# Performance work log

Measured on AMD Instinct MI355X. Metric: run time of the kernel, lower is better.

Reference implementation:

```python
import jax, jax.numpy as jnp
import numpy as np

LN_EPS = 1e-12


def setup_inputs() -> dict:
    key = jax.random.key(0)
    ks = jax.random.split(key, 10)
    B, S, W, D, H = 16, 512, 5, 200, 768
    std = 0.02
    return {
        "layer_output": jax.random.normal(ks[0], (B, S, H), dtype=jnp.float32),
        "word_embeddings": jax.random.normal(ks[1], (B, S, W, D), dtype=jnp.float32),
        "word_mask": jax.random.randint(ks[2], (B, S, W), 0, 2, dtype=jnp.int64),
        "W1": jax.random.normal(ks[3], (D, H), dtype=jnp.float32) * std,
        "b1": jnp.zeros((H,), dtype=jnp.float32),
        "W2": jax.random.normal(ks[4], (H, H), dtype=jnp.float32) * std,
        "b2": jnp.zeros((H,), dtype=jnp.float32),
        "attn_W": jax.random.normal(ks[5], (H, H), dtype=jnp.float32) * std,
        "ln_gamma": jnp.ones((H,), dtype=jnp.float32),
        "ln_beta": jnp.zeros((H,), dtype=jnp.float32),
    }


def reference(layer_output, word_embeddings, word_mask, W1, b1, W2, b2, attn_W, ln_gamma, ln_beta):
    # word_transform: Linear -> Tanh -> Linear (dropout = identity in eval)
    we = jnp.tanh(jnp.einsum("bswd,dh->bswh", word_embeddings, W1) + b1)
    we = jnp.einsum("bswh,hk->bswk", we, W2) + b2  # [B,S,W,H]

    # bilinear word attention: (x @ attn_W) . word_outputs -> score over W
    q = jnp.einsum("bsh,hk->bsk", layer_output, attn_W)  # [B,S,H]
    alpha = jnp.einsum("bsk,bswk->bsw", q, we)            # [B,S,W]
    alpha = alpha + (1.0 - word_mask.astype(alpha.dtype)) * -10000.0
    alpha = jax.nn.softmax(alpha, axis=-1)

    # weighted sum over words + residual
    agg = jnp.einsum("bsw,bswh->bsh", alpha, we)
    h = layer_output + agg

    # LayerNorm (fuse_layer; dropout = identity in eval)
    mu = jnp.mean(h, axis=-1, keepdims=True)
    var = jnp.mean(jnp.square(h - mu), axis=-1, keepdims=True)
    return (h - mu) * jax.lax.rsqrt(var + LN_EPS) * ln_gamma + ln_beta
```

## Files before the change

### kernel.cpp

```cpp
#include <hip/hip_runtime.h>
#include <hip/hip_bf16.h>
#include <math.h>


typedef __attribute__((ext_vector_type(8))) short bf16x8;
typedef __attribute__((ext_vector_type(4))) float f32x4;

__device__ __forceinline__ unsigned short f2bf_bits(float f) {
    __hip_bfloat16 h = __float2bfloat16(f);
    return *reinterpret_cast<unsigned short*>(&h);
}
__device__ __forceinline__ float bf_bits2f(unsigned short u) {
    union { unsigned int i; float f; } v; v.i = ((unsigned int)u) << 16; return v.f;
}
__device__ __forceinline__ float tanh_fast(float x) {
    float xc = fminf(fmaxf(x, -9.f), 9.f);
    float t  = __expf(2.f * xc);
    return (t - 1.f) * __builtin_amdgcn_rcpf(t + 1.f);
}
__device__ __forceinline__ bf16x8 pack8(float4 a, float4 b) {
    union { bf16x8 v; unsigned short s[8]; } u;
    u.s[0]=f2bf_bits(a.x); u.s[1]=f2bf_bits(a.y); u.s[2]=f2bf_bits(a.z); u.s[3]=f2bf_bits(a.w);
    u.s[4]=f2bf_bits(b.x); u.s[5]=f2bf_bits(b.y); u.s[6]=f2bf_bits(b.z); u.s[7]=f2bf_bits(b.w);
    return u.v;
}

__device__ __forceinline__ void async_cp16(const void* g, void* lds) {
#if __has_builtin(__builtin_amdgcn_global_load_lds)
    auto gp = (const __attribute__((address_space(1))) unsigned int*)g;
    auto lp = (__attribute__((address_space(3))) unsigned int*)lds;
    __builtin_amdgcn_global_load_lds(gp, lp, 16, 0, 0);
#else
    *(uint4*)lds = *(const uint4*)g;
#endif
}

__device__ __forceinline__ void sched_fence()  { asm volatile("" ::: "memory"); }
__device__ __forceinline__ void wait8_barrier(){ asm volatile("s_waitcnt vmcnt(8)\ns_barrier" ::: "memory"); }
__device__ __forceinline__ void wait0_barrier(){ asm volatile("s_waitcnt vmcnt(0)\ns_barrier" ::: "memory"); }
__device__ __forceinline__ void barrier_only() { asm volatile("s_barrier" ::: "memory"); }

template<bool F32SRC, bool HAS_BIAS, bool TANH_ACT, bool RESID, bool OUT_BF16,
         int N, int K, int KREAL>
__device__ __forceinline__ void gemm_body(
    const void* __restrict__ Ap, const void* __restrict__ Btp,
    const float* __restrict__ bias, const float* __restrict__ resid,
    void* __restrict__ outp, int m0, int n0, unsigned char* smem)
{
    constexpr int NIT = K / 64;
    const int tid  = threadIdx.x;
    const int lane = tid & 63;
    const int wave = tid >> 6;
    const int wm   = wave & 1;
    const int wn   = wave >> 1;
    const int row16 = lane & 15;
    const int kq    = lane >> 4;

    f32x4 acc[4][4];
#pragma unroll
    for (int i = 0; i < 4; i++)
#pragma unroll
        for (int j = 0; j < 4; j++) acc[i][j] = (f32x4){0.f, 0.f, 0.f, 0.f};

    auto compute_tile = [&](const unsigned short* As, const unsigned short* Bs, bool full) {
        bf16x8 af[2][4], bg[2][4];
#pragma unroll
        for (int mi = 0; mi < 4; mi++) {
            const int r = wm * 64 + mi * 16 + row16;
            af[0][mi] = *(const bf16x8*)&As[r * 64 + (kq ^ (r & 7)) * 8];
            if (full) af[1][mi] = *(const bf16x8*)&As[r * 64 + ((4 + kq) ^ (r & 7)) * 8];
        }
#pragma unroll
        for (int ni = 0; ni < 4; ni++) {
            const int r = wn * 64 + ni * 16 + row16;
            bg[0][ni] = *(const bf16x8*)&Bs[r * 64 + (kq ^ (r & 7)) * 8];
            if (full) bg[1][ni] = *(const bf16x8*)&Bs[r * 64 + ((4 + kq) ^ (r & 7)) * 8];
        }
        __builtin_amdgcn_s_setprio(1);
#pragma unroll
        for (int mi = 0; mi < 4; mi++)
#pragma unroll
            for (int ni = 0; ni < 4; ni++)
                acc[mi][ni] = __builtin_amdgcn_mfma_f32_16x16x32_bf16(
                    af[0][mi], bg[0][ni], acc[mi][ni], 0, 0, 0);
        if (full) {
#pragma unroll
            for (int mi = 0; mi < 4; mi++)
#pragma unroll
                for (int ni = 0; ni < 4; ni++)
                    acc[mi][ni] = __builtin_amdgcn_mfma_f32_16x16x32_bf16(
                        af[1][mi], bg[1][ni], acc[mi][ni], 0, 0, 0);
        }
        __builtin_amdgcn_s_setprio(0);
    };

    if constexpr (F32SRC) {
        const float* A32 = (const float*)Ap;
        const float* B32 = (const float*)Btp;
        unsigned short* As = (unsigned short*)smem;
        unsigned short* Bs = As + 8192;
        for (int t = 0; t < NIT; ++t) {
#pragma unroll
            for (int i = 0; i < 4; ++i) {
                const int c = i * 256 + tid;
                const int row = c >> 3, sl = c & 7;
                const int kcc = sl ^ (row & 7);
                const float* sa = A32 + (size_t)(m0 + row) * K + t * 64 + kcc * 8;
                *(bf16x8*)&As[row * 64 + sl * 8] = pack8(*(const float4*)sa, *(const float4*)(sa + 4));
                const float* sb = B32 + (size_t)(n0 + row) * K + t * 64 + kcc * 8;
                *(bf16x8*)&Bs[row * 64 + sl * 8] = pack8(*(const float4*)sb, *(const float4*)(sb + 4));
            }
            __syncthreads();
            compute_tile(As, Bs, true);
            __syncthreads();
        }
    } else {
        const __hip_bfloat16* A  = (const __hip_bfloat16*)Ap;
        const __hip_bfloat16* Bt = (const __hip_bfloat16*)Btp;
        const int rsub = lane >> 3;
        const int slot = lane & 7;
        const int kc   = slot ^ rsub;
        const __hip_bfloat16* gA = A  + (size_t)(m0 + wave * 32 + rsub) * K + kc * 8;
        const __hip_bfloat16* gB = Bt + (size_t)(n0 + wave * 32 + rsub) * K + kc * 8;
        unsigned short* lA0 = (unsigned short*)smem + wave * 2048 + lane * 8;
        unsigned short* lB0 = lA0 + 8192;

        auto stage = [&](int t, int buf) {
            unsigned short* lA = lA0 + buf * 16384;
            unsigned short* lB = lB0 + buf * 16384;
            const __hip_bfloat16* a = gA + t * 64;
            const __hip_bfloat16* b = gB + t * 64;
#pragma unroll
            for (int i = 0; i < 4; i++) {
                async_cp16(a + (size_t)(8 * i) * K, lA + i * 512);
                async_cp16(b + (size_t)(8 * i) * K, lB + i * 512);
            }
            sched_fence();
        };

        stage(0, 0);
        if (NIT > 1) stage(1, 1);
#pragma unroll
        for (int t = 0; t < NIT; ++t) {
            if (t == NIT - 1) wait0_barrier(); else wait8_barrier();
            const unsigned short* As = (const unsigned short*)(smem + (t & 1) * 32768);
            const unsigned short* Bs = As + 8192;
            compute_tile(As, Bs, (t * 64 + 32 < KREAL));
            barrier_only();
            if (t + 2 < NIT) stage(t + 2, t & 1);
        }
    }

    if (OUT_BF16) {
        unsigned short* rep = (unsigned short*)smem;
#pragma unroll
        for (int ni = 0; ni < 4; ni++) {
            const int c = wn * 64 + ni * 16 + row16;
            float bcol = HAS_BIAS ? bias[n0 + c] : 0.f;
#pragma unroll
            for (int mi = 0; mi < 4; mi++)
#pragma unroll
                for (int r = 0; r < 4; r++) {
                    const int rr = wm * 64 + mi * 16 + kq * 4 + r;
                    float v = acc[mi][ni][r];
                    if (HAS_BIAS) v += bcol;
                    if (TANH_ACT) v = tanh_fast(v);
                    rep[rr * 132 + c] = f2bf_bits(v);
                }
        }
        __syncthreads();
#pragma unroll
        for (int p = 0; p < 8; p++) {
            const int lin = p * 256 + tid;
            const int row = lin >> 4;
            const int c8  = lin & 15;
            const unsigned short* s = &rep[row * 132 + c8 * 8];
            union { uint4 u; unsigned long long q[2]; } d;
            d.q[0] = *(const unsigned long long*)(s);
            d.q[1] = *(const unsigned long long*)(s + 4);
            *(uint4*)((__hip_bfloat16*)outp + (size_t)(m0 + row) * N + n0 + c8 * 8) = d.u;
        }
    } else {
        float* rep = (float*)smem;
#pragma unroll
        for (int h = 0; h < 2; h++) {
            if (wm == h) {
#pragma unroll
                for (int ni = 0; ni < 4; ni++) {
                    const int c = wn * 64 + ni * 16 + row16;
                    float bcol = HAS_BIAS ? bias[n0 + c] : 0.f;
#pragma unroll
                    for (int mi = 0; mi < 4; mi++)
#pragma unroll
                        for (int r = 0; r < 4; r++) {
                            const int rr = mi * 16 + kq * 4 + r;
                            float v = acc[mi][ni][r];
                            if (HAS_BIAS) v += bcol;
                            if (TANH_ACT) v = tanh_fast(v);
                            rep[rr * 132 + c] = v;
                        }
                }
            }
            __syncthreads();
#pragma unroll
            for (int p = 0; p < 8; p++) {
                const int lin = p * 256 + tid;
                const int row = lin >> 5;
                const int c4  = lin & 31;
                float4 v = *(const float4*)&rep[row * 132 + c4 * 4];
                const int grow = m0 + h * 64 + row;
                if (RESID) {
                    float4 rv = *(const float4*)&resid[(size_t)grow * N + n0 + c4 * 4];
                    v.x += rv.x; v.y += rv.y; v.z += rv.z; v.w += rv.w;
                }
                *(float4*)((float*)outp + (size_t)grow * N + n0 + c4 * 4) = v;
            }
            __syncthreads();
        }
    }
}

template<bool HAS_BIAS, bool TANH_ACT, bool RESID, bool OUT_BF16, int N, int K, int GX>
__global__ __launch_bounds__(256) void mfma_gemm(
    const __hip_bfloat16* __restrict__ A,
    const __hip_bfloat16* __restrict__ Bt,
    const float* __restrict__ bias,
    const float* __restrict__ resid,
    void* __restrict__ outp)
{
    __shared__ __align__(16) unsigned char smem[65536];
    int bx, by;
    {
        const int total = gridDim.x;
        const int per_xcd = total >> 3;
        if ((total & 7) == 0 && (per_xcd % GX) == 0) {
            int xcd = blockIdx.x & 7, idx = blockIdx.x >> 3;
            int lin = xcd * per_xcd + idx;
            by = lin / GX; bx = lin % GX;
        } else { by = blockIdx.x / GX; bx = blockIdx.x % GX; }
    }
    gemm_body<false, HAS_BIAS, TANH_ACT, RESID, OUT_BF16, N, K, K>(
        A, Bt, bias, resid, outp, by * 128, bx * 128, smem);
}

__global__ __launch_bounds__(256) void tp_kernel(
    const __hip_bfloat16* __restrict__ Eb,  const __hip_bfloat16* __restrict__ W1Tb,
    const float* __restrict__ b1,           __hip_bfloat16* __restrict__ Tb,
    const __hip_bfloat16* __restrict__ xb,  const __hip_bfloat16* __restrict__ Ctb,
    __hip_bfloat16* __restrict__ Pb)
{
    __shared__ __align__(16) unsigned char smem[65536];
    if (blockIdx.x < 1920) {
        const int xcd = blockIdx.x & 7, idx = blockIdx.x >> 3;
        const int lin = xcd * 240 + idx;
        gemm_body<false, true, true, false, true, 768, 256, 224>(
            Eb, W1Tb, b1, nullptr, Tb, (lin / 6) * 128, (lin % 6) * 128, smem);
    } else {
        const int idq = blockIdx.x - 1920;
        const int xcd = idq & 7, idx = idq >> 3;
        const int lin = xcd * 48 + idx;
        gemm_body<false, false, false, false, true, 768, 768, 768>(
            xb, Ctb, nullptr, nullptr, Pb, (lin / 6) * 128, (lin % 6) * 128, smem);
    }
}

__global__ __launch_bounds__(256) void prep_kernel(
    const float* __restrict__ x,  __hip_bfloat16* __restrict__ xb,
    const float* __restrict__ w2,
    const float* __restrict__ aw,
    const float* __restrict__ E,  __hip_bfloat16* __restrict__ Eb,
    const float* __restrict__ W1, __hip_bfloat16* __restrict__ W1Tb,
    __hip_bfloat16* __restrict__ W2Tb,
    __hip_bfloat16* __restrict__ Ctb)
{
    __shared__ __align__(16) unsigned char smem[33792];
    float (*tile)[33] = (float(*)[33])smem;
    const int b = blockIdx.x, tid = threadIdx.x;
    if (b < 36) {
        gemm_body<true, false, false, false, true, 768, 768, 768>(
            w2, aw, nullptr, nullptr, Ctb, (b / 6) * 128, (b % 6) * 128, smem);
    } else if (b < 804) {
        const float* in; __hip_bfloat16* outb; int R, C, Rpad, t;
        if (b < 228) { t = b - 36;  in = W1; outb = W1Tb; R = 200; C = 768; Rpad = 256; }
        else         { t = b - 228; in = w2; outb = W2Tb; R = 768; C = 768; Rpad = 768; }
        const int c0 = (t % 24) * 32, r0 = (t / 24) * 32;
        const int xx = tid & 31, yy = tid >> 5;
#pragma unroll
        for (int i = 0; i < 32; i += 8) {
            int r = r0 + yy + i;
            tile[yy + i][xx] = (r < R) ? in[(size_t)r * C + c0 + xx] : 0.f;
        }
        __syncthreads();
#pragma unroll
        for (int i = 0; i < 32; i += 8)
            outb[(size_t)(c0 + yy + i) * Rpad + r0 + xx] = __float2bfloat16(tile[xx][yy + i]);
    } else if (b < 1572) {
        const long long base = (long long)(b - 804) * 2048 + tid;
        float4 v[8];
#pragma unroll
        for (int j = 0; j < 8; j++) v[j] = ((const float4*)x)[base + j * 256];
#pragma unroll
        for (int j = 0; j < 8; j++)
            ((ushort4*)xb)[base + j * 256] =
                make_ushort4(f2bf_bits(v[j].x), f2bf_bits(v[j].y), f2bf_bits(v[j].z), f2bf_bits(v[j].w));
    } else {
        const int lane = tid & 63, wave = tid >> 6;
        const long long r0 = (long long)(b - 1572) * 32 + wave * 8;
        const int k = lane * 4;
        float4 v[8];
#pragma unroll
        for (int j = 0; j < 8; j++) {
            v[j] = make_float4(0.f, 0.f, 0.f, 0.f);
            if (k < 200) v[j] = *(const float4*)&E[(r0 + j) * 200 + k];
        }
#pragma unroll
        for (int j = 0; j < 8; j++)
            *(ushort4*)&Eb[(r0 + j) * 256 + k] =
                make_ushort4(f2bf_bits(v[j].x), f2bf_bits(v[j].y), f2bf_bits(v[j].z), f2bf_bits(v[j].w));
    }
}

__global__ __launch_bounds__(256) void attn_kernel(
    const __hip_bfloat16* __restrict__ T,
    const __hip_bfloat16* P,
    const int* __restrict__ mask,
    __hip_bfloat16* S)
{
    const int lane = threadIdx.x & 63;
    const int wave = threadIdx.x >> 6;
    const int r    = blockIdx.x * 4 + wave;
    const int base = lane * 12;

    float pv[12];
    {
        const ushort4* pp = (const ushort4*)((const unsigned short*)P + (size_t)r * 768 + base);
        ushort4 u0 = pp[0], u1 = pp[1], u2 = pp[2];
        unsigned short us[12] = {u0.x,u0.y,u0.z,u0.w, u1.x,u1.y,u1.z,u1.w, u2.x,u2.y,u2.z,u2.w};
#pragma unroll
        for (int j = 0; j < 12; j++) pv[j] = bf_bits2f(us[j]);
    }
    float tv[5][12], part[5];
#pragma unroll
    for (int w = 0; w < 5; w++) {
        const ushort4* tp = (const ushort4*)((const unsigned short*)T + ((size_t)r * 5 + w) * 768 + base);
        ushort4 u0 = tp[0], u1 = tp[1], u2 = tp[2];
        unsigned short us[12] = {u0.x,u0.y,u0.z,u0.w, u1.x,u1.y,u1.z,u1.w, u2.x,u2.y,u2.z,u2.w};
        float s = 0.f;
#pragma unroll
        for (int j = 0; j < 12; j++) { tv[w][j] = bf_bits2f(us[j]); s += tv[w][j] * pv[j]; }
        part[w] = s;
    }
#pragma unroll
    for (int off = 32; off > 0; off >>= 1)
#pragma unroll
        for (int w = 0; w < 5; w++)
            part[w] += __shfl_xor(part[w], off, 64);

    float logit[5], mx = -1e30f;
#pragma unroll
    for (int w = 0; w < 5; w++) {
        float m = (float)mask[(size_t)r * 5 + w];
        logit[w] = part[w] - 10000.0f * (1.0f - m);
        mx = fmaxf(mx, logit[w]);
    }
    float se = 0.f;
#pragma unroll
    for (int w = 0; w < 5; w++) { logit[w] = expf(logit[w] - mx); se += logit[w]; }
    const float inv = 1.0f / se;

    unsigned short os[12];
#pragma unroll
    for (int j = 0; j < 12; j++) {
        float s = 0.f;
#pragma unroll
        for (int w = 0; w < 5; w++) s += logit[w] * tv[w][j];
        os[j] = f2bf_bits(s * inv);
    }
    ushort4* sp = (ushort4*)((unsigned short*)S + (size_t)r * 768 + base);
    sp[0] = make_ushort4(os[0], os[1], os[2],  os[3]);
    sp[1] = make_ushort4(os[4], os[5], os[6],  os[7]);
    sp[2] = make_ushort4(os[8], os[9], os[10], os[11]);
}

__global__ __launch_bounds__(256) void ln_kernel(
    const float* __restrict__ Hbuf, const float* __restrict__ gamma,
    const float* __restrict__ beta, float* __restrict__ out)
{
    const int lane = threadIdx.x & 63;
    const int wave = threadIdx.x >> 6;
    const int r    = blockIdx.x * 4 + wave;
    const float* hr = Hbuf + (size_t)r * 768 + lane * 12;

    float v[12];
    {
        float4 a = *(const float4*)(hr);
        float4 b = *(const float4*)(hr + 4);
        float4 c = *(const float4*)(hr + 8);
        v[0]=a.x; v[1]=a.y; v[2]=a.z; v[3]=a.w;
        v[4]=b.x; v[5]=b.y; v[6]=b.z; v[7]=b.w;
        v[8]=c.x; v[9]=c.y; v[10]=c.z; v[11]=c.w;
    }
    float s = 0.f;
#pragma unroll
    for (int j = 0; j < 12; j++) s += v[j];
#pragma unroll
    for (int off = 32; off > 0; off >>= 1) s += __shfl_xor(s, off, 64);
    const float mu = s * (1.f / 768.f);
    float vs = 0.f;
#pragma unroll
    for (int j = 0; j < 12; j++) { float d = v[j] - mu; vs += d * d; }
#pragma unroll
    for (int off = 32; off > 0; off >>= 1) vs += __shfl_xor(vs, off, 64);
    const float rs = rsqrtf(vs * (1.f / 768.f) + 1e-12f);

    float o[12];
#pragma unroll
    for (int j = 0; j < 12; j++) {
        int h = lane * 12 + j;
        o[j] = (v[j] - mu) * rs * gamma[h] + beta[h];
    }
    float* orow = out + (size_t)r * 768 + lane * 12;
    *(float4*)(orow)     = make_float4(o[0], o[1], o[2],  o[3]);
    *(float4*)(orow + 4) = make_float4(o[4], o[5], o[6],  o[7]);
    *(float4*)(orow + 8) = make_float4(o[8], o[9], o[10], o[11]);
}

extern "C" void kernel_launch(void* const* d_in, const int* in_sizes, int n_in,
                              void* d_out, int out_size, void* d_ws, size_t ws_size,
                              hipStream_t stream)
{
    const float* x      = (const float*)d_in[0];
    const float* E      = (const float*)d_in[1];
    const int*   mask   = (const int*)d_in[2];
    const float* W1     = (const float*)d_in[3];
    const float* b1     = (const float*)d_in[4];
    const float* W2     = (const float*)d_in[5];
    const float* b2     = (const float*)d_in[6];
    const float* attn_W = (const float*)d_in[7];
    const float* gamma  = (const float*)d_in[8];
    const float* beta   = (const float*)d_in[9];
    float* out = (float*)d_out;

    const int BS = 8192, H = 768, M1 = 40960, KP = 256;

    char* p = (char*)d_ws;
    auto alloc = [&](size_t bytes) { char* q = p; p += (bytes + 255) & ~(size_t)255; return q; };
    __hip_bfloat16* xb    = (__hip_bfloat16*)alloc((size_t)BS * H * 2);
    __hip_bfloat16* W2Tb  = (__hip_bfloat16*)alloc((size_t)H * H * 2);
    __hip_bfloat16* Ctb   = (__hip_bfloat16*)alloc((size_t)H * H * 2);
    __hip_bfloat16* W1Tb  = (__hip_bfloat16*)alloc((size_t)H * KP * 2);
    __hip_bfloat16* Tb    = (__hip_bfloat16*)alloc((size_t)M1 * H * 2);
    __hip_bfloat16* Eb    = (__hip_bfloat16*)alloc((size_t)M1 * KP * 2);
    __hip_bfloat16* Pb    = (__hip_bfloat16*)alloc((size_t)BS * H * 2);
    float* Hb = (float*)Tb;
    __hip_bfloat16* Sb = Pb;

    prep_kernel<<<2852, 256, 0, stream>>>(x, xb, W2, attn_W, E, Eb, W1, W1Tb, W2Tb, Ctb);

    tp_kernel<<<2304, 256, 0, stream>>>(Eb, W1Tb, b1, Tb, xb, Ctb, Pb);

    attn_kernel<<<BS / 4, 256, 0, stream>>>(Tb, Pb, mask, Sb);

    mfma_gemm<true, false, true, false, 768, 768, 6><<<384, 256, 0, stream>>>(
        Sb, W2Tb, b2, x, Hb);

    ln_kernel<<<BS / 4, 256, 0, stream>>>(Hb, gamma, beta, out);
}
```

Before: 212.7 us.

## Use 256x128 tiles with 512-thread blocks for bf16 GEMMs

Adds a 512-thread GEMM body that computes 256x128 output tiles with eight waves and a double-buffered async LDS load of 96 KB. The T/P GEMMs and the final H GEMM are moved onto it, halving block counts. The f32-source path is split into its own simplified body. The larger tiles are meant to improve reuse of the B tile and cut load traffic, at the cost of more LDS per block and lower occupancy. The H GEMM now launches only 192 blocks, which can leave compute units idle.

```diff
diff --git a/kernel.cpp b/kernel.cpp
--- a/kernel.cpp
+++ b/kernel.cpp
@@ -36,7 +36,7 @@
 }
 
 __device__ __forceinline__ void sched_fence()  { asm volatile("" ::: "memory"); }
-__device__ __forceinline__ void wait8_barrier(){ asm volatile("s_waitcnt vmcnt(8)\ns_barrier" ::: "memory"); }
+__device__ __forceinline__ void wait6_barrier(){ asm volatile("s_waitcnt vmcnt(6)\ns_barrier" ::: "memory"); }
 __device__ __forceinline__ void wait0_barrier(){ asm volatile("s_waitcnt vmcnt(0)\ns_barrier" ::: "memory"); }
 __device__ __forceinline__ void barrier_only() { asm volatile("s_barrier" ::: "memory"); }
 
@@ -62,7 +62,130 @@
 #pragma unroll
         for (int j = 0; j < 4; j++) acc[i][j] = (f32x4){0.f, 0.f, 0.f, 0.f};
 
-    auto compute_tile = [&](const unsigned short* As, const unsigned short* Bs, bool full) {
+    const float* A32 = (const float*)Ap;
+    const float* B32 = (const float*)Btp;
+    unsigned short* As = (unsigned short*)smem;
+    unsigned short* Bs = As + 8192;
+    for (int t = 0; t < NIT; ++t) {
+#pragma unroll
+        for (int i = 0; i < 4; ++i) {
+            const int c = i * 256 + tid;
+            const int row = c >> 3, sl = c & 7;
+            const int kcc = sl ^ (row & 7);
+            const float* sa = A32 + (size_t)(m0 + row) * K + t * 64 + kcc * 8;
+            *(bf16x8*)&As[row * 64 + sl * 8] = pack8(*(const float4*)sa, *(const float4*)(sa + 4));
+            const float* sb = B32 + (size_t)(n0 + row) * K + t * 64 + kcc * 8;
+            *(bf16x8*)&Bs[row * 64 + sl * 8] = pack8(*(const float4*)sb, *(const float4*)(sb + 4));
+        }
+        __syncthreads();
+        bf16x8 af[2][4], bg[2][4];
+#pragma unroll
+        for (int mi = 0; mi < 4; mi++) {
+            const int r = wm * 64 + mi * 16 + row16;
+            af[0][mi] = *(const bf16x8*)&As[r * 64 + (kq ^ (r & 7)) * 8];
+            af[1][mi] = *(const bf16x8*)&As[r * 64 + ((4 + kq) ^ (r & 7)) * 8];
+        }
+#pragma unroll
+        for (int ni = 0; ni < 4; ni++) {
+            const int r = wn * 64 + ni * 16 + row16;
+            bg[0][ni] = *(const bf16x8*)&Bs[r * 64 + (kq ^ (r & 7)) * 8];
+            bg[1][ni] = *(const bf16x8*)&Bs[r * 64 + ((4 + kq) ^ (r & 7)) * 8];
+        }
+#pragma unroll
+        for (int h = 0; h < 2; h++)
+#pragma unroll
+            for (int mi = 0; mi < 4; mi++)
+#pragma unroll
+                for (int ni = 0; ni < 4; ni++)
+                    acc[mi][ni] = __builtin_amdgcn_mfma_f32_16x16x32_bf16(
+                        af[h][mi], bg[h][ni], acc[mi][ni], 0, 0, 0);
+        __syncthreads();
+    }
+
+    unsigned short* rep = (unsigned short*)smem;
+#pragma unroll
+    for (int ni = 0; ni < 4; ni++) {
+        const int c = wn * 64 + ni * 16 + row16;
+        float bcol = HAS_BIAS ? bias[n0 + c] : 0.f;
+#pragma unroll
+        for (int mi = 0; mi < 4; mi++)
+#pragma unroll
+            for (int r = 0; r < 4; r++) {
+                const int rr = wm * 64 + mi * 16 + kq * 4 + r;
+                float v = acc[mi][ni][r];
+                if (HAS_BIAS) v += bcol;
+                if (TANH_ACT) v = tanh_fast(v);
+                rep[rr * 132 + c] = f2bf_bits(v);
+            }
+    }
+    __syncthreads();
+#pragma unroll
+    for (int p = 0; p < 8; p++) {
+        const int lin = p * 256 + tid;
+        const int row = lin >> 4;
+        const int c8  = lin & 15;
+        const unsigned short* s = &rep[row * 132 + c8 * 8];
+        union { uint4 u; unsigned long long q[2]; } d;
+        d.q[0] = *(const unsigned long long*)(s);
+        d.q[1] = *(const unsigned long long*)(s + 4);
+        *(uint4*)((__hip_bfloat16*)outp + (size_t)(m0 + row) * N + n0 + c8 * 8) = d.u;
+    }
+}
+
+template<bool HAS_BIAS, bool TANH_ACT, bool RESID, bool OUT_BF16, int N, int K, int KREAL>
+__device__ __forceinline__ void gemm_body512(
+    const __hip_bfloat16* __restrict__ A,
+    const __hip_bfloat16* __restrict__ Bt,
+    const float* __restrict__ bias,
+    const float* __restrict__ resid,
+    void* __restrict__ outp,
+    int m0, int n0, unsigned char* smem)
+{
+    constexpr int NIT = K / 64;
+    const int tid  = threadIdx.x;
+    const int lane = tid & 63;
+    const int wave = tid >> 6;
+    const int wm   = wave & 3;
+    const int wn   = wave >> 2;
+    const int row16 = lane & 15;
+    const int kq    = lane >> 4;
+
+    f32x4 acc[4][4];
+#pragma unroll
+    for (int i = 0; i < 4; i++)
+#pragma unroll
+        for (int j = 0; j < 4; j++) acc[i][j] = (f32x4){0.f, 0.f, 0.f, 0.f};
+
+    auto stage = [&](int t, int buf) {
+        unsigned short* Ab = (unsigned short*)(smem + buf * 49152);
+        unsigned short* Bb = Ab + 16384;
+#pragma unroll
+        for (int i = 0; i < 4; i++) {
+            const int c = i * 512 + tid;
+            const int row = c >> 3, sl = c & 7;
+            const int kcc = sl ^ (row & 7);
+            async_cp16(A + (size_t)(m0 + row) * K + t * 64 + kcc * 8, Ab + c * 8);
+        }
+#pragma unroll
+        for (int i = 0; i < 2; i++) {
+            const int c = i * 512 + tid;
+            const int row = c >> 3, sl = c & 7;
+            const int kcc = sl ^ (row & 7);
+            async_cp16(Bt + (size_t)(n0 + row) * K + t * 64 + kcc * 8, Bb + c * 8);
+        }
+        sched_fence();
+    };
+
+    stage(0, 0);
+    stage(1, 1);
+#pragma unroll
+    for (int t = 0; t < NIT; ++t) {
+        if (t == NIT - 1) wait0_barrier(); else wait6_barrier();
+
+        const unsigned short* As = (const unsigned short*)(smem + (t & 1) * 49152);
+        const unsigned short* Bs = As + 16384;
+        const bool full = (t * 64 + 32 < KREAL);
+
         bf16x8 af[2][4], bg[2][4];
 #pragma unroll
         for (int mi = 0; mi < 4; mi++) {
@@ -92,98 +215,49 @@
                         af[1][mi], bg[1][ni], acc[mi][ni], 0, 0, 0);
         }
         __builtin_amdgcn_s_setprio(0);
-    };
-
-    if constexpr (F32SRC) {
-        const float* A32 = (const float*)Ap;
-        const float* B32 = (const float*)Btp;
-        unsigned short* As = (unsigned short*)smem;
-        unsigned short* Bs = As + 8192;
-        for (int t = 0; t < NIT; ++t) {
-#pragma unroll
-            for (int i = 0; i < 4; ++i) {
-                const int c = i * 256 + tid;
-                const int row = c >> 3, sl = c & 7;
-                const int kcc = sl ^ (row & 7);
-                const float* sa = A32 + (size_t)(m0 + row) * K + t * 64 + kcc * 8;
-                *(bf16x8*)&As[row * 64 + sl * 8] = pack8(*(const float4*)sa, *(const float4*)(sa + 4));
-                const float* sb = B32 + (size_t)(n0 + row) * K + t * 64 + kcc * 8;
-                *(bf16x8*)&Bs[row * 64 + sl * 8] = pack8(*(const float4*)sb, *(const float4*)(sb + 4));
+        barrier_only();
+        if (t + 2 < NIT) stage(t + 2, t & 1);
+    }
+
+    if (OUT_BF16) {
+        unsigned short* rep = (unsigned short*)smem;
+#pragma unroll
+        for (int h = 0; h < 2; h++) {
+            if ((wm >> 1) == h) {
+#pragma unroll
+                for (int ni = 0; ni < 4; ni++) {
+                    const int c = wn * 64 + ni * 16 + row16;
+                    float bcol = HAS_BIAS ? bias[n0 + c] : 0.f;
+#pragma unroll
+                    for (int mi = 0; mi < 4; mi++)
+#pragma unroll
+                        for (int r = 0; r < 4; r++) {
+                            const int rr = (wm & 1) * 64 + mi * 16 + kq * 4 + r;
+                            float v = acc[mi][ni][r];
+                            if (HAS_BIAS) v += bcol;
+                            if (TANH_ACT) v = tanh_fast(v);
+                            rep[rr * 132 + c] = f2bf_bits(v);
+                        }
+                }
             }
             __syncthreads();
-            compute_tile(As, Bs, true);
+#pragma unroll
+            for (int p = 0; p < 4; p++) {
+                const int lin = p * 512 + tid;
+                const int row = lin >> 4;
+                const int c8  = lin & 15;
+                const unsigned short* s = &rep[row * 132 + c8 * 8];
+                union { uint4 u; unsigned long long q[2]; } d;
+                d.q[0] = *(const unsigned long long*)(s);
+                d.q[1] = *(const unsigned long long*)(s + 4);
+                *(uint4*)((__hip_bfloat16*)outp + (size_t)(m0 + h * 128 + row) * N + n0 + c8 * 8) = d.u;
+            }
             __syncthreads();
-        }
-    } else {
-        const __hip_bfloat16* A  = (const __hip_bfloat16*)Ap;
-        const __hip_bfloat16* Bt = (const __hip_bfloat16*)Btp;
-        const int rsub = lane >> 3;
-        const int slot = lane & 7;
-        const int kc   = slot ^ rsub;
-        const __hip_bfloat16* gA = A  + (size_t)(m0 + wave * 32 + rsub) * K + kc * 8;
-        const __hip_bfloat16* gB = Bt + (size_t)(n0 + wave * 32 + rsub) * K + kc * 8;
-        unsigned short* lA0 = (unsigned short*)smem + wave * 2048 + lane * 8;
-        unsigned short* lB0 = lA0 + 8192;
-
-        auto stage = [&](int t, int buf) {
-            unsigned short* lA = lA0 + buf * 16384;
-            unsigned short* lB = lB0 + buf * 16384;
-            const __hip_bfloat16* a = gA + t * 64;
-            const __hip_bfloat16* b = gB + t * 64;
-#pragma unroll
-            for (int i = 0; i < 4; i++) {
-                async_cp16(a + (size_t)(8 * i) * K, lA + i * 512);
-                async_cp16(b + (size_t)(8 * i) * K, lB + i * 512);
-            }
-            sched_fence();
-        };
-
-        stage(0, 0);
-        if (NIT > 1) stage(1, 1);
-#pragma unroll
-        for (int t = 0; t < NIT; ++t) {
-            if (t == NIT - 1) wait0_barrier(); else wait8_barrier();
-            const unsigned short* As = (const unsigned short*)(smem + (t & 1) * 32768);
-            const unsigned short* Bs = As + 8192;
-            compute_tile(As, Bs, (t * 64 + 32 < KREAL));
-            barrier_only();
-            if (t + 2 < NIT) stage(t + 2, t & 1);
-        }
-    }
-
-    if (OUT_BF16) {
-        unsigned short* rep = (unsigned short*)smem;
-#pragma unroll
-        for (int ni = 0; ni < 4; ni++) {
-            const int c = wn * 64 + ni * 16 + row16;
-            float bcol = HAS_BIAS ? bias[n0 + c] : 0.f;
-#pragma unroll
-            for (int mi = 0; mi < 4; mi++)
-#pragma unroll
-                for (int r = 0; r < 4; r++) {
-                    const int rr = wm * 64 + mi * 16 + kq * 4 + r;
-                    float v = acc[mi][ni][r];
-                    if (HAS_BIAS) v += bcol;
-                    if (TANH_ACT) v = tanh_fast(v);
-                    rep[rr * 132 + c] = f2bf_bits(v);
-                }
-        }
-        __syncthreads();
-#pragma unroll
-        for (int p = 0; p < 8; p++) {
-            const int lin = p * 256 + tid;
-            const int row = lin >> 4;
-            const int c8  = lin & 15;
-            const unsigned short* s = &rep[row * 132 + c8 * 8];
-            union { uint4 u; unsigned long long q[2]; } d;
-            d.q[0] = *(const unsigned long long*)(s);
-            d.q[1] = *(const unsigned long long*)(s + 4);
-            *(uint4*)((__hip_bfloat16*)outp + (size_t)(m0 + row) * N + n0 + c8 * 8) = d.u;
         }
     } else {
         float* rep = (float*)smem;
 #pragma unroll
-        for (int h = 0; h < 2; h++) {
+        for (int h = 0; h < 4; h++) {
             if (wm == h) {
 #pragma unroll
                 for (int ni = 0; ni < 4; ni++) {
@@ -203,8 +277,8 @@
             }
             __syncthreads();
 #pragma unroll
-            for (int p = 0; p < 8; p++) {
-                const int lin = p * 256 + tid;
+            for (int p = 0; p < 4; p++) {
+                const int lin = p * 512 + tid;
                 const int row = lin >> 5;
                 const int c4  = lin & 31;
                 float4 v = *(const float4*)&rep[row * 132 + c4 * 4];
@@ -220,48 +294,37 @@
     }
 }
 
-template<bool HAS_BIAS, bool TANH_ACT, bool RESID, bool OUT_BF16, int N, int K, int GX>
-__global__ __launch_bounds__(256) void mfma_gemm(
-    const __hip_bfloat16* __restrict__ A,
-    const __hip_bfloat16* __restrict__ Bt,
-    const float* __restrict__ bias,
-    const float* __restrict__ resid,
-    void* __restrict__ outp)
-{
-    __shared__ __align__(16) unsigned char smem[65536];
-    int bx, by;
-    {
-        const int total = gridDim.x;
-        const int per_xcd = total >> 3;
-        if ((total & 7) == 0 && (per_xcd % GX) == 0) {
-            int xcd = blockIdx.x & 7, idx = blockIdx.x >> 3;
-            int lin = xcd * per_xcd + idx;
-            by = lin / GX; bx = lin % GX;
-        } else { by = blockIdx.x / GX; bx = blockIdx.x % GX; }
-    }
-    gemm_body<false, HAS_BIAS, TANH_ACT, RESID, OUT_BF16, N, K, K>(
-        A, Bt, bias, resid, outp, by * 128, bx * 128, smem);
-}
-
-__global__ __launch_bounds__(256) void tp_kernel(
+__global__ __launch_bounds__(512) void tp_kernel(
     const __hip_bfloat16* __restrict__ Eb,  const __hip_bfloat16* __restrict__ W1Tb,
     const float* __restrict__ b1,           __hip_bfloat16* __restrict__ Tb,
     const __hip_bfloat16* __restrict__ xb,  const __hip_bfloat16* __restrict__ Ctb,
     __hip_bfloat16* __restrict__ Pb)
 {
-    __shared__ __align__(16) unsigned char smem[65536];
-    if (blockIdx.x < 1920) {
+    __shared__ __align__(16) unsigned char smem[98304];
+    if (blockIdx.x < 960) {
         const int xcd = blockIdx.x & 7, idx = blockIdx.x >> 3;
-        const int lin = xcd * 240 + idx;
-        gemm_body<false, true, true, false, true, 768, 256, 224>(
-            Eb, W1Tb, b1, nullptr, Tb, (lin / 6) * 128, (lin % 6) * 128, smem);
+        const int lin = xcd * 120 + idx;
+        gemm_body512<true, true, false, true, 768, 256, 224>(
+            Eb, W1Tb, b1, nullptr, Tb, (lin / 6) * 256, (lin % 6) * 128, smem);
     } else {
-        const int idq = blockIdx.x - 1920;
+        const int idq = blockIdx.x - 960;
         const int xcd = idq & 7, idx = idq >> 3;
-        const int lin = xcd * 48 + idx;
-        gemm_body<false, false, false, false, true, 768, 768, 768>(
-            xb, Ctb, nullptr, nullptr, Pb, (lin / 6) * 128, (lin % 6) * 128, smem);
-    }
+        const int lin = xcd * 24 + idx;
+        gemm_body512<false, false, false, true, 768, 768, 768>(
+            xb, Ctb, nullptr, nullptr, Pb, (lin / 6) * 256, (lin % 6) * 128, smem);
+    }
+}
+
+__global__ __launch_bounds__(512) void hgemm_kernel(
+    const __hip_bfloat16* __restrict__ Sb,  const __hip_bfloat16* __restrict__ W2Tb,
+    const float* __restrict__ b2,           const float* __restrict__ x,
+    float* __restrict__ Hb)
+{
+    __shared__ __align__(16) unsigned char smem[98304];
+    const int xcd = blockIdx.x & 7, idx = blockIdx.x >> 3;
+    const int lin = xcd * 24 + idx;
+    gemm_body512<true, false, true, false, 768, 768, 768>(
+        Sb, W2Tb, b2, x, Hb, (lin / 6) * 256, (lin % 6) * 128, smem);
 }
 
 __global__ __launch_bounds__(256) void prep_kernel(
@@ -457,12 +520,11 @@
 
     prep_kernel<<<2852, 256, 0, stream>>>(x, xb, W2, attn_W, E, Eb, W1, W1Tb, W2Tb, Ctb);
 
-    tp_kernel<<<2304, 256, 0, stream>>>(Eb, W1Tb, b1, Tb, xb, Ctb, Pb);
+    tp_kernel<<<1152, 512, 0, stream>>>(Eb, W1Tb, b1, Tb, xb, Ctb, Pb);
 
     attn_kernel<<<BS / 4, 256, 0, stream>>>(Tb, Pb, mask, Sb);
 
-    mfma_gemm<true, false, true, false, 768, 768, 6><<<384, 256, 0, stream>>>(
-        Sb, W2Tb, b2, x, Hb);
+    hgemm_kernel<<<192, 512, 0, stream>>>(Sb, W2Tb, b2, x, Hb);
 
     ln_kernel<<<BS / 4, 256, 0, stream>>>(Hb, gamma, beta, out);
 }
```

Result: slower. 238.8 us (+12.3%).
